# Performance work log

Hardware: AMD Instinct MI355X
Metric: run time of the kernel (lower is better)

## Reference

```python
import jax, jax.numpy as jnp
import numpy as np

LATENT = 256; INPUT = 128; NUNITS = 256; DEC_OUT = 128
NTRAJ = 256; NTP = 512
INTERP = 2  # hard-coded in the original forward

def _mlp_sig(x, w1, b1, w2, b2):
    return jax.nn.sigmoid(jnp.tanh(x @ w1 + b1) @ w2 + b2)

def _mlp_lin(x, w1, b1, w2, b2):
    return jnp.tanh(x @ w1 + b1) @ w2 + b2

def _gru_step(y, yt, x, ug, ugt, rg, ns):
    # x: [N, 2*INPUT]; first half = features, second half = observation mask channels
    xh = x[:, :INPUT]
    yc = jnp.concatenate([y, xh], axis=-1)                 # [N, LATENT+INPUT]
    u = _mlp_sig(yc, *ug)
    ut = _mlp_sig(yc, *ugt)
    r = _mlp_sig(yc, *rg)
    new_state = _mlp_lin(jnp.concatenate([y * r, xh], axis=-1), *ns)
    new_y = (1.0 - u) * new_state + u * y
    new_yt = (1.0 - ut) * new_state + ut * yt
    mask = (jnp.sum(x[:, INPUT:], axis=-1, keepdims=True) > 0).astype(x.dtype)
    return mask * new_y + (1.0 - mask) * y, mask * new_yt + (1.0 - mask) * yt

def setup_inputs():
    key = jax.random.key(0)
    ks = iter(jax.random.split(key, 32))
    def p(shape):
        return jax.random.normal(next(ks), shape, dtype=jnp.float32) * 0.05
    d = {}
    d["data"] = jax.random.normal(next(ks), (NTRAJ, NTP, 2 * INPUT), dtype=jnp.float32)
    dts = jax.random.uniform(next(ks), (NTRAJ, NTP), dtype=jnp.float32) + 0.1
    d["time_steps"] = jnp.cumsum(dts, axis=1)              # strictly increasing times
    gin = LATENT + INPUT
    for name in ("ug", "ugt", "rg", "rgt", "ns"):
        d[name + "_w1"] = p((gin, NUNITS)); d[name + "_b1"] = jnp.zeros((NUNITS,), jnp.float32)
        d[name + "_w2"] = p((NUNITS, LATENT)); d[name + "_b2"] = jnp.zeros((LATENT,), jnp.float32)
    d["dk_w1"] = p((LATENT, LATENT)); d["dk_b1"] = jnp.zeros((LATENT,), jnp.float32)
    d["dk_w2"] = p((LATENT, 1)); d["dk_b2"] = jnp.zeros((1,), jnp.float32)
    d["dec_w"] = p((LATENT, DEC_OUT)); d["dec_b"] = jnp.zeros((DEC_OUT,), jnp.float32)
    return d

def reference(data, time_steps,
              ug_w1, ug_b1, ug_w2, ug_b2,
              ugt_w1, ugt_b1, ugt_w2, ugt_b2,
              rg_w1, rg_b1, rg_w2, rg_b2,
              rgt_w1, rgt_b1, rgt_w2, rgt_b2,
              ns_w1, ns_b1, ns_w2, ns_b2,
              dk_w1, dk_b1, dk_w2, dk_b2,
              dec_w, dec_b):
    # Note: reset_gate_target (rgt_*) is computed but never used in the original forward.
    ug = (ug_w1, ug_b1, ug_w2, ug_b2)
    ugt = (ugt_w1, ugt_b1, ugt_w2, ugt_b2)
    rg = (rg_w1, rg_b1, rg_w2, rg_b2)
    ns = (ns_w1, ns_b1, ns_w2, ns_b2)
    n_traj = data.shape[0]
    lin = jnp.linspace(0.0, 1.0, INTERP + 1, dtype=data.dtype)  # [3]
    y0 = jnp.zeros((n_traj, LATENT), data.dtype)
    # step i=0: no decay interpolation, yi_decay = prev_y (zeros)
    y, yt = _gru_step(y0, y0, data[:, 0, :], ug, ugt, rg, ns)
    dts = time_steps[:, 1:] - time_steps[:, :-1]                # [N, T-1]
    xs = jnp.moveaxis(data[:, 1:, :], 1, 0)                     # [T-1, N, 2I]

    def step(carry, inp):
        y, yt = carry
        x, dt = inp
        decay = jax.nn.relu(jax.nn.relu(y @ dk_w1 + dk_b1) @ dk_w2 + dk_b2)  # [N,1]
        e = jnp.exp(-decay * (dt[:, None] * lin[None, :]))                   # [N,3]
        ydec = yt[:, None, :] + (y - yt)[:, None, :] * e[:, :, None]         # [N,3,L]
        vol = jnp.mean(ydec[:, :-1, :] @ dec_w + dec_b, axis=-2)             # [N,D]
        y2, yt2 = _gru_step(ydec[:, -1, :], yt, x, ug, ugt, rg, ns)
        return (y2, yt2), vol

    (y, yt), vols = jax.lax.scan(step, (y, yt), (xs, dts.T))
    prev_y = y[None, :, :]                       # [1, N, L]
    volume_dt = jnp.transpose(vols, (1, 0, 2))   # [N, T-1, D]
    return prev_y, volume_dt, dts
```

## Files before the change

### kernel.cpp

```cpp
#include <hip/hip_runtime.h>
#include <hip/hip_fp16.h>

#define NTRAJ   256
#define NTP     512
#define NSTEPS  511
#define LATENT  256
#define INPUT   128
#define DEC_OUT 128

#define OUT_VOL ((size_t)NTRAJ * LATENT)
#define OUT_DTS (OUT_VOL + (size_t)NTRAJ * NSTEPS * DEC_OUT)

#define WU_UG1  0
#define WU_UG2  49152
#define WU_UGT1 81920
#define WU_UGT2 131072
#define WU_RG1  163840
#define WU_RG2  212992
#define WU_NS1  245760
#define WU_NS2  294912
#define WU_DK1  327680
#define WU_DEC  360448
#define WU_TOT  376832

typedef _Float16 h2_t __attribute__((ext_vector_type(2)));
union U32H2 { unsigned int u; h2_t h; };

__device__ __forceinline__ float dot2f(unsigned int wu, unsigned int xu, float acc) {
#if defined(__has_builtin) && __has_builtin(__builtin_amdgcn_fdot2)
    U32H2 a, b; a.u = wu; b.u = xu;
    return __builtin_amdgcn_fdot2(a.h, b.h, acc, false);
#else
    U32H2 a, b; a.u = wu; b.u = xu;
    return acc + (float)a.h.x * (float)b.h.x + (float)a.h.y * (float)b.h.y;
#endif
}

__device__ __forceinline__ float wred(float v) {
    #pragma unroll
    for (int off = 32; off; off >>= 1) v += __shfl_down(v, off, 64);
    return v;
}
__device__ __forceinline__ float fast_sigmoid(float x) { return 1.0f / (1.0f + __expf(-x)); }
__device__ __forceinline__ float fast_tanh(float x) {
    float e = __expf(2.0f * x);
    return 1.0f - 2.0f / (e + 1.0f);
}
__device__ __forceinline__ unsigned int packpair(float v) {
    float vn = __shfl_xor(v, 1, 64);
    U32H2 r; r.h.x = (_Float16)v; r.h.y = (_Float16)vn;
    return r.u;
}

extern "C" __global__ void __launch_bounds__(256)
convert_w(const float* __restrict__ ug_w1, const float* __restrict__ ug_w2,
          const float* __restrict__ ugt_w1, const float* __restrict__ ugt_w2,
          const float* __restrict__ rg_w1, const float* __restrict__ rg_w2,
          const float* __restrict__ ns_w1, const float* __restrict__ ns_w2,
          const float* __restrict__ dk_w1, const float* __restrict__ dec_w,
          unsigned int* __restrict__ ws)
{
    const int i = blockIdx.x * 256 + threadIdx.x;
    const float* s; int o; int cbits;
    if      (i < WU_UG2)  { s = ug_w1;  o = i;           cbits = 8; }
    else if (i < WU_UGT1) { s = ug_w2;  o = i - WU_UG2;  cbits = 8; }
    else if (i < WU_UGT2) { s = ugt_w1; o = i - WU_UGT1; cbits = 8; }
    else if (i < WU_RG1)  { s = ugt_w2; o = i - WU_UGT2; cbits = 8; }
    else if (i < WU_RG2)  { s = rg_w1;  o = i - WU_RG1;  cbits = 8; }
    else if (i < WU_NS1)  { s = rg_w2;  o = i - WU_RG2;  cbits = 8; }
    else if (i < WU_NS2)  { s = ns_w1;  o = i - WU_NS1;  cbits = 8; }
    else if (i < WU_DK1)  { s = ns_w2;  o = i - WU_NS2;  cbits = 8; }
    else if (i < WU_DEC)  { s = dk_w1;  o = i - WU_DK1;  cbits = 8; }
    else                  { s = dec_w;  o = i - WU_DEC;  cbits = 7; }
    const int C  = 1 << cbits;
    const int kp = o >> cbits;
    const int c  = o & (C - 1);
    const float v0 = s[(2 * kp) * C + c];
    const float v1 = s[(2 * kp + 1) * C + c];
    const unsigned int h0 = __half_as_ushort(__float2half(v0));
    const unsigned int h1 = __half_as_ushort(__float2half(v1));
    ws[i] = h0 | (h1 << 16);
}

extern "C" __global__ void __launch_bounds__(512, 2)
rnn_decay_kernel3(const float* __restrict__ data, const float* __restrict__ ts,
                  const float* __restrict__ ug_b1, const float* __restrict__ ug_b2,
                  const float* __restrict__ ugt_b1, const float* __restrict__ ugt_b2,
                  const float* __restrict__ rg_b1, const float* __restrict__ rg_b2,
                  const float* __restrict__ ns_b1, const float* __restrict__ ns_b2,
                  const float* __restrict__ dk_b1, const float* __restrict__ dk_w2,
                  const float* __restrict__ dk_b2, const float* __restrict__ dec_b,
                  const unsigned int* __restrict__ wsu, float* __restrict__ out)
{
    __shared__ __align__(16) float s_part[8192];
    __shared__ unsigned int s_in_h[192];
    __shared__ unsigned int s_ns_h[192];
    __shared__ unsigned int s_y_h[128];
    __shared__ unsigned int s_a_h[128];
    __shared__ unsigned int s_b_h[128];
    __shared__ unsigned int s_c_h[128];
    __shared__ unsigned int s_v_h[128];
    __shared__ float s_ut[256];
    __shared__ float s_red[8];

    const int tid  = threadIdx.x;
    const int w    = tid >> 6;
    const int lane = tid & 63;
    const int c    = tid & 255;
    const int cl4  = lane << 2;
    const int traj = blockIdx.x;

    const unsigned int* UG1  = wsu + WU_UG1;  const unsigned int* UG2  = wsu + WU_UG2;
    const unsigned int* UGT1 = wsu + WU_UGT1; const unsigned int* UGT2 = wsu + WU_UGT2;
    const unsigned int* RG1  = wsu + WU_RG1;  const unsigned int* RG2  = wsu + WU_RG2;
    const unsigned int* NS1  = wsu + WU_NS1;  const unsigned int* NS2  = wsu + WU_NS2;
    const unsigned int* DK1  = wsu + WU_DK1;  const unsigned int* DECW = wsu + WU_DEC;

    const float* dbase = data + (size_t)traj * NTP * (2 * INPUT);
    const float* tbase = ts + (size_t)traj * NTP;
    float* vol_out = out + OUT_VOL + (size_t)traj * NSTEPS * DEC_OUT;
    float* dts_out = out + OUT_DTS + (size_t)traj * NSTEPS;

    if (tid < 256)
        for (int t = c; t < NSTEPS; t += 256)
            dts_out[t] = tbase[t + 1] - tbase[t];

    float r_y = 0.f, r_yt = 0.f;

    for (int t = -1; t < NSTEPS; ++t) {
        const bool first = (t < 0);

        if (tid < 256) {
            const float xv = first ? dbase[c] : dbase[(size_t)(t + 1) * 256 + c];
            float mv = (c >= 128) ? xv : 0.f;
            mv = wred(mv);
            if (lane == 0) s_red[w] = mv;
            if (c < 128) {
                const unsigned int px = packpair(xv);
                if (!(lane & 1)) { s_in_h[128 + (c >> 1)] = px; s_ns_h[128 + (c >> 1)] = px; }
            }
            if (first && !(lane & 1)) s_in_h[c >> 1] = 0u;
        }

        float r_ydec = 0.f, r_u = 0.f, r_r = 0.f;
        bool maskv;

        if (!first) {
            float4 aD = make_float4(0, 0, 0, 0);
            const int kp0 = w << 4;
            #pragma unroll 4
            for (int i = 0; i < 16; ++i) {
                const unsigned int x = s_y_h[kp0 + i];
                const uint4 wv = *(const uint4*)(DK1 + (size_t)(kp0 + i) * 256 + cl4);
                aD.x = dot2f(wv.x, x, aD.x); aD.y = dot2f(wv.y, x, aD.y);
                aD.z = dot2f(wv.z, x, aD.z); aD.w = dot2f(wv.w, x, aD.w);
            }
            *(float4*)(s_part + (w << 8) + cl4) = aD;
            __syncthreads();
            if (tid < 256) {
                float v = dk_b1[c];
                #pragma unroll
                for (int i = 0; i < 8; ++i) v += s_part[(i << 8) + c];
                v = fmaxf(v, 0.f);
                float pv = wred(v * dk_w2[c]);
                if (lane == 0) s_red[4 + w] = pv;
            }
            __syncthreads();
            const float decay = fmaxf(s_red[4] + s_red[5] + s_red[6] + s_red[7] + dk_b2[0], 0.f);
            maskv = (s_red[0] + s_red[1] + s_red[2] + s_red[3]) > 0.f;
            if (tid < 256) {
                const float dt = tbase[t + 1] - tbase[t];
                const float diff = r_y - r_yt;
                const float ef = __expf(-decay * dt);
                const float eh = __expf(-0.5f * decay * dt);
                r_ydec = r_yt + diff * ef;
                const float vol = 0.5f * (r_y + r_yt + diff * eh);
                const unsigned int pd = packpair(r_ydec);
                const unsigned int pvv = packpair(vol);
                if (!(lane & 1)) { s_in_h[c >> 1] = pd; s_v_h[c >> 1] = pvv; }
            }
            __syncthreads();
        } else {
            __syncthreads();
            maskv = (s_red[0] + s_red[1] + s_red[2] + s_red[3]) > 0.f;
        }

        if (!first) {
            float4 aE = make_float4(0, 0, 0, 0);
            const int hh = lane >> 5, cl = (lane & 31) << 2;
            const int kpb = (w << 4) + hh;
            #pragma unroll 4
            for (int i = 0; i < 8; ++i) {
                const int kp = kpb + (i << 1);
                const uint4 wv = *(const uint4*)(DECW + (size_t)kp * 128 + cl);
                const unsigned int x = s_v_h[kp];
                aE.x = dot2f(wv.x, x, aE.x); aE.y = dot2f(wv.y, x, aE.y);
                aE.z = dot2f(wv.z, x, aE.z); aE.w = dot2f(wv.w, x, aE.w);
            }
            *(float4*)(s_part + 6144 + ((w << 1) + hh) * 128 + cl) = aE;
        }
        {
            float4 aA = make_float4(0, 0, 0, 0), aB = aA, aC = aA;
            const int kp0 = w * 24;
            #pragma unroll 4
            for (int i = 0; i < 24; ++i) {
                const int kp = kp0 + i;
                const unsigned int x = s_in_h[kp];
                const uint4 wa = *(const uint4*)(UG1  + (size_t)kp * 256 + cl4);
                const uint4 wb = *(const uint4*)(UGT1 + (size_t)kp * 256 + cl4);
                const uint4 wc = *(const uint4*)(RG1  + (size_t)kp * 256 + cl4);
                aA.x = dot2f(wa.x, x, aA.x); aA.y = dot2f(wa.y, x, aA.y);
                aA.z = dot2f(wa.z, x, aA.z); aA.w = dot2f(wa.w, x, aA.w);
                aB.x = dot2f(wb.x, x, aB.x); aB.y = dot2f(wb.y, x, aB.y);
                aB.z = dot2f(wb.z, x, aB.z); aB.w = dot2f(wb.w, x, aB.w);
                aC.x = dot2f(wc.x, x, aC.x); aC.y = dot2f(wc.y, x, aC.y);
                aC.z = dot2f(wc.z, x, aC.z); aC.w = dot2f(wc.w, x, aC.w);
            }
            *(float4*)(s_part + (w << 8) + cl4)          = aA;
            *(float4*)(s_part + 2048 + (w << 8) + cl4)   = aB;
            *(float4*)(s_part + 4096 + (w << 8) + cl4)   = aC;
        }
        __syncthreads();
        {
            const int s = tid >> 8;
            float v = (s ? ugt_b1 : ug_b1)[c];
            const float* pb = s_part + (s ? 2048 : 0) + c;
            #pragma unroll
            for (int i = 0; i < 8; ++i) v += pb[i << 8];
            v = fast_tanh(v);
            const unsigned int pk = packpair(v);
            if (!(lane & 1)) (s ? s_b_h : s_a_h)[c >> 1] = pk;
            if (tid < 256) {
                float v2 = rg_b1[c];
                const float* pb2 = s_part + 4096 + c;
                #pragma unroll
                for (int i = 0; i < 8; ++i) v2 += pb2[i << 8];
                v2 = fast_tanh(v2);
                const unsigned int pk2 = packpair(v2);
                if (!(lane & 1)) s_c_h[c >> 1] = pk2;
            }
            if (!first && tid < 128) {
                float vd = dec_b[tid];
                const float* pbd = s_part + 6144 + tid;
                #pragma unroll
                for (int i = 0; i < 16; ++i) vd += pbd[i << 7];
                vol_out[(size_t)t * DEC_OUT + tid] = vd;
            }
        }
        __syncthreads();

        {
            float4 aA = make_float4(0, 0, 0, 0), aB = aA, aC = aA;
            const int kp0 = w << 4;
            #pragma unroll 4
            for (int i = 0; i < 16; ++i) {
                const int kp = kp0 + i;
                const unsigned int xa = s_a_h[kp];
                const unsigned int xb = s_b_h[kp];
                const unsigned int xc = s_c_h[kp];
                const uint4 wa = *(const uint4*)(UG2  + (size_t)kp * 256 + cl4);
                const uint4 wb = *(const uint4*)(UGT2 + (size_t)kp * 256 + cl4);
                const uint4 wc = *(const uint4*)(RG2  + (size_t)kp * 256 + cl4);
                aA.x = dot2f(wa.x, xa, aA.x); aA.y = dot2f(wa.y, xa, aA.y);
                aA.z = dot2f(wa.z, xa, aA.z); aA.w = dot2f(wa.w, xa, aA.w);
                aB.x = dot2f(wb.x, xb, aB.x); aB.y = dot2f(wb.y, xb, aB.y);
                aB.z = dot2f(wb.z, xb, aB.z); aB.w = dot2f(wb.w, xb, aB.w);
                aC.x = dot2f(wc.x, xc, aC.x); aC.y = dot2f(wc.y, xc, aC.y);
                aC.z = dot2f(wc.z, xc, aC.z); aC.w = dot2f(wc.w, xc, aC.w);
            }
            *(float4*)(s_part + (w << 8) + cl4)          = aA;
            *(float4*)(s_part + 2048 + (w << 8) + cl4)   = aB;
            *(float4*)(s_part + 4096 + (w << 8) + cl4)   = aC;
        }
        __syncthreads();
        {
            const int s = tid >> 8;
            float v = (s ? ugt_b2 : ug_b2)[c];
            const float* pb = s_part + (s ? 2048 : 0) + c;
            #pragma unroll
            for (int i = 0; i < 8; ++i) v += pb[i << 8];
            v = fast_sigmoid(v);
            if (s) s_ut[c] = v; else r_u = v;
            if (tid < 256) {
                float v2 = rg_b2[c];
                const float* pb2 = s_part + 4096 + c;
                #pragma unroll
                for (int i = 0; i < 8; ++i) v2 += pb2[i << 8];
                r_r = fast_sigmoid(v2);
                const unsigned int pk = packpair(r_ydec * r_r);
                if (!(lane & 1)) s_ns_h[c >> 1] = pk;
            }
        }
        __syncthreads();

        {
            float4 aA = make_float4(0, 0, 0, 0);
            const int kp0 = w * 24;
            #pragma unroll 4
            for (int i = 0; i < 24; ++i) {
                const int kp = kp0 + i;
                const unsigned int x = s_ns_h[kp];
                const uint4 wa = *(const uint4*)(NS1 + (size_t)kp * 256 + cl4);
                aA.x = dot2f(wa.x, x, aA.x); aA.y = dot2f(wa.y, x, aA.y);
                aA.z = dot2f(wa.z, x, aA.z); aA.w = dot2f(wa.w, x, aA.w);
            }
            *(float4*)(s_part + (w << 8) + cl4) = aA;
        }
        __syncthreads();
        if (tid < 256) {
            float v = ns_b1[c];
            #pragma unroll
            for (int i = 0; i < 8; ++i) v += s_part[(i << 8) + c];
            v = fast_tanh(v);
            const unsigned int pk = packpair(v);
            if (!(lane & 1)) s_a_h[c >> 1] = pk;
        }
        __syncthreads();

        {
            float4 aA = make_float4(0, 0, 0, 0);
            const int kp0 = w << 4;
            #pragma unroll 4
            for (int i = 0; i < 16; ++i) {
                const int kp = kp0 + i;
                const unsigned int x = s_a_h[kp];
                const uint4 wa = *(const uint4*)(NS2 + (size_t)kp * 256 + cl4);
                aA.x = dot2f(wa.x, x, aA.x); aA.y = dot2f(wa.y, x, aA.y);
                aA.z = dot2f(wa.z, x, aA.z); aA.w = dot2f(wa.w, x, aA.w);
            }
            *(float4*)(s_part + (w << 8) + cl4) = aA;
        }
        __syncthreads();
        if (tid < 256) {
            float nsv = ns_b2[c];
            #pragma unroll
            for (int i = 0; i < 8; ++i) nsv += s_part[(i << 8) + c];
            const float u = r_u, ut = s_ut[c];
            const float ny  = (1.f - u)  * nsv + u  * r_ydec;
            const float nyt = (1.f - ut) * nsv + ut * r_yt;
            r_y  = maskv ? ny  : r_ydec;
            r_yt = maskv ? nyt : r_yt;
            const unsigned int pk = packpair(r_y);
            if (!(lane & 1)) s_y_h[c >> 1] = pk;
        }
        __syncthreads();
    }

    if (tid < 256)
        out[(size_t)traj * 256 + c] = r_y;
}

extern "C" void kernel_launch(void* const* d_in, const int* in_sizes, int n_in,
                              void* d_out, int out_size, void* d_ws, size_t ws_size,
                              hipStream_t stream) {
    const float* data   = (const float*)d_in[0];
    const float* ts     = (const float*)d_in[1];
    const float* ug_w1  = (const float*)d_in[2];
    const float* ug_b1  = (const float*)d_in[3];
    const float* ug_w2  = (const float*)d_in[4];
    const float* ug_b2  = (const float*)d_in[5];
    const float* ugt_w1 = (const float*)d_in[6];
    const float* ugt_b1 = (const float*)d_in[7];
    const float* ugt_w2 = (const float*)d_in[8];
    const float* ugt_b2 = (const float*)d_in[9];
    const float* rg_w1  = (const float*)d_in[10];
    const float* rg_b1  = (const float*)d_in[11];
    const float* rg_w2  = (const float*)d_in[12];
    const float* rg_b2  = (const float*)d_in[13];
    const float* ns_w1  = (const float*)d_in[18];
    const float* ns_b1  = (const float*)d_in[19];
    const float* ns_w2  = (const float*)d_in[20];
    const float* ns_b2  = (const float*)d_in[21];
    const float* dk_w1  = (const float*)d_in[22];
    const float* dk_b1  = (const float*)d_in[23];
    const float* dk_w2  = (const float*)d_in[24];
    const float* dk_b2  = (const float*)d_in[25];
    const float* dec_w  = (const float*)d_in[26];
    const float* dec_b  = (const float*)d_in[27];

    unsigned int* wsu = (unsigned int*)d_ws;

    convert_w<<<WU_TOT / 256, 256, 0, stream>>>(ug_w1, ug_w2, ugt_w1, ugt_w2,
                                                rg_w1, rg_w2, ns_w1, ns_w2,
                                                dk_w1, dec_w, wsu);

    rnn_decay_kernel3<<<NTRAJ, 512, 0, stream>>>(
        data, ts, ug_b1, ug_b2, ugt_b1, ugt_b2, rg_b1, rg_b2, ns_b1, ns_b2,
        dk_b1, dk_w2, dk_b2, dec_b, wsu, (float*)d_out);
}
```

Baseline: 7.585 ms.

## Replace shared-memory partial reductions with intra-wave shuffle reductions per output column

Each matvec is now split so each wave owns 32 output columns and its 8 lane groups split the K dimension. Partial sums are combined with xor-shuffle butterflies instead of being written to a 32KB shared scratch array and re-summed. This removes the separate reduction phases and about half of the __syncthreads per timestep, and frees a large shared buffer. In exchange it adds shuffle traffic, and the activation work after each reduction is done redundantly by every lane group rather than spread across threads.

Result: slower. 8.042 ms (+6.0%).

```diff
diff --git a/kernel.cpp b/kernel.cpp
--- a/kernel.cpp
+++ b/kernel.cpp
@@ -50,6 +50,16 @@
     float vn = __shfl_xor(v, 1, 64);
     U32H2 r; r.h.x = (_Float16)v; r.h.y = (_Float16)vn;
     return r.u;
+}
+__device__ __forceinline__ unsigned int pk2(float a, float b) {
+    U32H2 r; r.h.x = (_Float16)a; r.h.y = (_Float16)b; return r.u;
+}
+__device__ __forceinline__ float4 bfly4(float4 v, int m) {
+    v.x += __shfl_xor(v.x, m, 64);
+    v.y += __shfl_xor(v.y, m, 64);
+    v.z += __shfl_xor(v.z, m, 64);
+    v.w += __shfl_xor(v.w, m, 64);
+    return v;
 }
 
 extern "C" __global__ void __launch_bounds__(256)
@@ -82,8 +92,12 @@
     ws[i] = h0 | (h1 << 16);
 }
 
+#define DOT1(acc, wv, xv) { \
+    acc.x = dot2f((wv).x, (xv), acc.x); acc.y = dot2f((wv).y, (xv), acc.y); \
+    acc.z = dot2f((wv).z, (xv), acc.z); acc.w = dot2f((wv).w, (xv), acc.w); }
+
 extern "C" __global__ void __launch_bounds__(512, 2)
-rnn_decay_kernel3(const float* __restrict__ data, const float* __restrict__ ts,
+rnn_decay_kernel4(const float* __restrict__ data, const float* __restrict__ ts,
                   const float* __restrict__ ug_b1, const float* __restrict__ ug_b2,
                   const float* __restrict__ ugt_b1, const float* __restrict__ ugt_b2,
                   const float* __restrict__ rg_b1, const float* __restrict__ rg_b2,
@@ -92,22 +106,25 @@
                   const float* __restrict__ dk_b2, const float* __restrict__ dec_b,
                   const unsigned int* __restrict__ wsu, float* __restrict__ out)
 {
-    __shared__ __align__(16) float s_part[8192];
-    __shared__ unsigned int s_in_h[192];
-    __shared__ unsigned int s_ns_h[192];
-    __shared__ unsigned int s_y_h[128];
-    __shared__ unsigned int s_a_h[128];
-    __shared__ unsigned int s_b_h[128];
-    __shared__ unsigned int s_c_h[128];
-    __shared__ unsigned int s_v_h[128];
-    __shared__ float s_ut[256];
-    __shared__ float s_red[8];
+    __shared__ __align__(16) unsigned int s_in_h[192];
+    __shared__ __align__(16) unsigned int s_ns_h[192];
+    __shared__ __align__(16) unsigned int s_y_h[128];
+    __shared__ __align__(16) unsigned int s_a_h[128];
+    __shared__ __align__(16) unsigned int s_b_h[128];
+    __shared__ __align__(16) unsigned int s_c_h[128];
+    __shared__ __align__(16) unsigned int s_v_h[128];
+    __shared__ float s_red[12];
 
     const int tid  = threadIdx.x;
     const int w    = tid >> 6;
     const int lane = tid & 63;
     const int c    = tid & 255;
-    const int cl4  = lane << 2;
+    const int sl   = lane >> 3;
+    const int g    = lane & 7;
+    const int c0   = (w << 5) + (g << 2);
+    const int h2b  = c0 >> 1;
+    const int sld  = lane >> 2;
+    const int c0d  = (w << 4) + ((lane & 3) << 2);
     const int traj = blockIdx.x;
 
     const unsigned int* UG1  = wsu + WU_UG1;  const unsigned int* UG2  = wsu + WU_UG2;
@@ -122,232 +139,225 @@
     float* dts_out = out + OUT_DTS + (size_t)traj * NSTEPS;
 
     if (tid < 256)
-        for (int t = c; t < NSTEPS; t += 256)
-            dts_out[t] = tbase[t + 1] - tbase[t];
-
-    float r_y = 0.f, r_yt = 0.f;
+        for (int t0 = c; t0 < NSTEPS; t0 += 256)
+            dts_out[t0] = tbase[t0 + 1] - tbase[t0];
+
+    const float4 ugb1v  = *(const float4*)(ug_b1  + c0);
+    const float4 ugtb1v = *(const float4*)(ugt_b1 + c0);
+    const float4 rgb1v  = *(const float4*)(rg_b1  + c0);
+    const float4 nsb1v  = *(const float4*)(ns_b1  + c0);
+    const float4 ugb2v  = *(const float4*)(ug_b2  + c0);
+    const float4 ugtb2v = *(const float4*)(ugt_b2 + c0);
+    const float4 rgb2v  = *(const float4*)(rg_b2  + c0);
+    const float4 nsb2v  = *(const float4*)(ns_b2  + c0);
+    const float4 dkb1v  = *(const float4*)(dk_b1  + c0);
+    const float4 dkw2v  = *(const float4*)(dk_w2  + c0);
+    const float4 decbv  = *(const float4*)(dec_b  + c0d);
+    const float  dkb2s  = dk_b2[0];
+
+    float4 y4  = make_float4(0.f, 0.f, 0.f, 0.f);
+    float4 yt4 = y4;
 
     for (int t = -1; t < NSTEPS; ++t) {
         const bool first = (t < 0);
 
+        float dt_t = 0.f;
+        if (!first) dt_t = tbase[t + 1] - tbase[t];
+        float xval = 0.f;
+        if (tid < 256)
+            xval = first ? dbase[c] : dbase[(size_t)(t + 1) * 256 + c];
+
+        if (!first) {
+            float4 aD = make_float4(0.f, 0.f, 0.f, 0.f);
+            #pragma unroll 4
+            for (int i = 0; i < 16; ++i) {
+                const int kp = sl + (i << 3);
+                const unsigned int xv = s_y_h[kp];
+                const uint4 wv = *(const uint4*)(DK1 + (size_t)kp * 256 + c0);
+                DOT1(aD, wv, xv);
+            }
+            aD = bfly4(aD, 8); aD = bfly4(aD, 16); aD = bfly4(aD, 32);
+            float sdk = fmaxf(aD.x + dkb1v.x, 0.f) * dkw2v.x
+                      + fmaxf(aD.y + dkb1v.y, 0.f) * dkw2v.y
+                      + fmaxf(aD.z + dkb1v.z, 0.f) * dkw2v.z
+                      + fmaxf(aD.w + dkb1v.w, 0.f) * dkw2v.w;
+            sdk += __shfl_xor(sdk, 1, 64);
+            sdk += __shfl_xor(sdk, 2, 64);
+            sdk += __shfl_xor(sdk, 4, 64);
+            if (lane == 0) s_red[4 + w] = sdk;
+        }
         if (tid < 256) {
-            const float xv = first ? dbase[c] : dbase[(size_t)(t + 1) * 256 + c];
-            float mv = (c >= 128) ? xv : 0.f;
+            float mv = (c >= 128) ? xval : 0.f;
             mv = wred(mv);
             if (lane == 0) s_red[w] = mv;
             if (c < 128) {
-                const unsigned int px = packpair(xv);
+                const unsigned int px = packpair(xval);
                 if (!(lane & 1)) { s_in_h[128 + (c >> 1)] = px; s_ns_h[128 + (c >> 1)] = px; }
             }
             if (first && !(lane & 1)) s_in_h[c >> 1] = 0u;
         }
-
-        float r_ydec = 0.f, r_u = 0.f, r_r = 0.f;
-        bool maskv;
-
+        __syncthreads();
+
+        const bool maskv = (s_red[0] + s_red[1] + s_red[2] + s_red[3]) > 0.f;
+        float4 ydec4 = make_float4(0.f, 0.f, 0.f, 0.f);
         if (!first) {
-            float4 aD = make_float4(0, 0, 0, 0);
-            const int kp0 = w << 4;
+            const float decay = fmaxf(s_red[4] + s_red[5] + s_red[6] + s_red[7]
+                                    + s_red[8] + s_red[9] + s_red[10] + s_red[11]
+                                    + dkb2s, 0.f);
+            const float ef = __expf(-decay * dt_t);
+            const float eh = __expf(-0.5f * decay * dt_t);
+            float4 vol4;
+            ydec4.x = yt4.x + (y4.x - yt4.x) * ef;
+            ydec4.y = yt4.y + (y4.y - yt4.y) * ef;
+            ydec4.z = yt4.z + (y4.z - yt4.z) * ef;
+            ydec4.w = yt4.w + (y4.w - yt4.w) * ef;
+            vol4.x = 0.5f * (y4.x + yt4.x + (y4.x - yt4.x) * eh);
+            vol4.y = 0.5f * (y4.y + yt4.y + (y4.y - yt4.y) * eh);
+            vol4.z = 0.5f * (y4.z + yt4.z + (y4.z - yt4.z) * eh);
+            vol4.w = 0.5f * (y4.w + yt4.w + (y4.w - yt4.w) * eh);
+            if (!sl) {
+                uint2 pd; pd.x = pk2(ydec4.x, ydec4.y); pd.y = pk2(ydec4.z, ydec4.w);
+                uint2 pv; pv.x = pk2(vol4.x, vol4.y);   pv.y = pk2(vol4.z, vol4.w);
+                *(uint2*)(s_in_h + h2b) = pd;
+                *(uint2*)(s_v_h + h2b)  = pv;
+            }
+        }
+        __syncthreads();
+
+        if (!first) {
+            float4 aE = make_float4(0.f, 0.f, 0.f, 0.f);
+            #pragma unroll 4
+            for (int i = 0; i < 8; ++i) {
+                const int kp = sld + (i << 4);
+                const unsigned int xv = s_v_h[kp];
+                const uint4 wv = *(const uint4*)(DECW + (size_t)kp * 128 + c0d);
+                DOT1(aE, wv, xv);
+            }
+            aE = bfly4(aE, 4); aE = bfly4(aE, 8); aE = bfly4(aE, 16); aE = bfly4(aE, 32);
+            if (sld == 0) {
+                float4 o;
+                o.x = aE.x + decbv.x; o.y = aE.y + decbv.y;
+                o.z = aE.z + decbv.z; o.w = aE.w + decbv.w;
+                *(float4*)(vol_out + (size_t)t * DEC_OUT + c0d) = o;
+            }
+        }
+        {
+            float4 aA = make_float4(0.f, 0.f, 0.f, 0.f), aB = aA, aC = aA;
+            #pragma unroll 4
+            for (int i = 0; i < 24; ++i) {
+                const int kp = sl + (i << 3);
+                const unsigned int xv = s_in_h[kp];
+                const uint4 wa = *(const uint4*)(UG1  + (size_t)kp * 256 + c0);
+                const uint4 wb = *(const uint4*)(UGT1 + (size_t)kp * 256 + c0);
+                const uint4 wc = *(const uint4*)(RG1  + (size_t)kp * 256 + c0);
+                DOT1(aA, wa, xv); DOT1(aB, wb, xv); DOT1(aC, wc, xv);
+            }
+            aA = bfly4(aA, 8); aA = bfly4(aA, 16); aA = bfly4(aA, 32);
+            aB = bfly4(aB, 8); aB = bfly4(aB, 16); aB = bfly4(aB, 32);
+            aC = bfly4(aC, 8); aC = bfly4(aC, 16); aC = bfly4(aC, 32);
+            if (!sl) {
+                uint2 pa, pb, pc;
+                pa.x = pk2(fast_tanh(aA.x + ugb1v.x),  fast_tanh(aA.y + ugb1v.y));
+                pa.y = pk2(fast_tanh(aA.z + ugb1v.z),  fast_tanh(aA.w + ugb1v.w));
+                pb.x = pk2(fast_tanh(aB.x + ugtb1v.x), fast_tanh(aB.y + ugtb1v.y));
+                pb.y = pk2(fast_tanh(aB.z + ugtb1v.z), fast_tanh(aB.w + ugtb1v.w));
+                pc.x = pk2(fast_tanh(aC.x + rgb1v.x),  fast_tanh(aC.y + rgb1v.y));
+                pc.y = pk2(fast_tanh(aC.z + rgb1v.z),  fast_tanh(aC.w + rgb1v.w));
+                *(uint2*)(s_a_h + h2b) = pa;
+                *(uint2*)(s_b_h + h2b) = pb;
+                *(uint2*)(s_c_h + h2b) = pc;
+            }
+        }
+        __syncthreads();
+
+        float4 u4, ut4;
+        {
+            float4 aA = make_float4(0.f, 0.f, 0.f, 0.f), aB = aA, aC = aA;
             #pragma unroll 4
             for (int i = 0; i < 16; ++i) {
-                const unsigned int x = s_y_h[kp0 + i];
-                const uint4 wv = *(const uint4*)(DK1 + (size_t)(kp0 + i) * 256 + cl4);
-                aD.x = dot2f(wv.x, x, aD.x); aD.y = dot2f(wv.y, x, aD.y);
-                aD.z = dot2f(wv.z, x, aD.z); aD.w = dot2f(wv.w, x, aD.w);
-            }
-            *(float4*)(s_part + (w << 8) + cl4) = aD;
-            __syncthreads();
-            if (tid < 256) {
-                float v = dk_b1[c];
-                #pragma unroll
-                for (int i = 0; i < 8; ++i) v += s_part[(i << 8) + c];
-                v = fmaxf(v, 0.f);
-                float pv = wred(v * dk_w2[c]);
-                if (lane == 0) s_red[4 + w] = pv;
-            }
-            __syncthreads();
-            const float decay = fmaxf(s_red[4] + s_red[5] + s_red[6] + s_red[7] + dk_b2[0], 0.f);
-            maskv = (s_red[0] + s_red[1] + s_red[2] + s_red[3]) > 0.f;
-            if (tid < 256) {
-                const float dt = tbase[t + 1] - tbase[t];
-                const float diff = r_y - r_yt;
-                const float ef = __expf(-decay * dt);
-                const float eh = __expf(-0.5f * decay * dt);
-                r_ydec = r_yt + diff * ef;
-                const float vol = 0.5f * (r_y + r_yt + diff * eh);
-                const unsigned int pd = packpair(r_ydec);
-                const unsigned int pvv = packpair(vol);
-                if (!(lane & 1)) { s_in_h[c >> 1] = pd; s_v_h[c >> 1] = pvv; }
-            }
-            __syncthreads();
-        } else {
-            __syncthreads();
-            maskv = (s_red[0] + s_red[1] + s_red[2] + s_red[3]) > 0.f;
-        }
-
-        if (!first) {
-            float4 aE = make_float4(0, 0, 0, 0);
-            const int hh = lane >> 5, cl = (lane & 31) << 2;
-            const int kpb = (w << 4) + hh;
-            #pragma unroll 4
-            for (int i = 0; i < 8; ++i) {
-                const int kp = kpb + (i << 1);
-                const uint4 wv = *(const uint4*)(DECW + (size_t)kp * 128 + cl);
-                const unsigned int x = s_v_h[kp];
-                aE.x = dot2f(wv.x, x, aE.x); aE.y = dot2f(wv.y, x, aE.y);
-                aE.z = dot2f(wv.z, x, aE.z); aE.w = dot2f(wv.w, x, aE.w);
-            }
-            *(float4*)(s_part + 6144 + ((w << 1) + hh) * 128 + cl) = aE;
-        }
-        {
-            float4 aA = make_float4(0, 0, 0, 0), aB = aA, aC = aA;
-            const int kp0 = w * 24;
-            #pragma unroll 4
-            for (int i = 0; i < 24; ++i) {
-                const int kp = kp0 + i;
-                const unsigned int x = s_in_h[kp];
-                const uint4 wa = *(const uint4*)(UG1  + (size_t)kp * 256 + cl4);
-                const uint4 wb = *(const uint4*)(UGT1 + (size_t)kp * 256 + cl4);
-                const uint4 wc = *(const uint4*)(RG1  + (size_t)kp * 256 + cl4);
-                aA.x = dot2f(wa.x, x, aA.x); aA.y = dot2f(wa.y, x, aA.y);
-                aA.z = dot2f(wa.z, x, aA.z); aA.w = dot2f(wa.w, x, aA.w);
-                aB.x = dot2f(wb.x, x, aB.x); aB.y = dot2f(wb.y, x, aB.y);
-                aB.z = dot2f(wb.z, x, aB.z); aB.w = dot2f(wb.w, x, aB.w);
-                aC.x = dot2f(wc.x, x, aC.x); aC.y = dot2f(wc.y, x, aC.y);
-                aC.z = dot2f(wc.z, x, aC.z); aC.w = dot2f(wc.w, x, aC.w);
-            }
-            *(float4*)(s_part + (w << 8) + cl4)          = aA;
-            *(float4*)(s_part + 2048 + (w << 8) + cl4)   = aB;
-            *(float4*)(s_part + 4096 + (w << 8) + cl4)   = aC;
-        }
-        __syncthreads();
-        {
-            const int s = tid >> 8;
-            float v = (s ? ugt_b1 : ug_b1)[c];
-            const float* pb = s_part + (s ? 2048 : 0) + c;
-            #pragma unroll
-            for (int i = 0; i < 8; ++i) v += pb[i << 8];
-            v = fast_tanh(v);
-            const unsigned int pk = packpair(v);
-            if (!(lane & 1)) (s ? s_b_h : s_a_h)[c >> 1] = pk;
-            if (tid < 256) {
-                float v2 = rg_b1[c];
-                const float* pb2 = s_part + 4096 + c;
-                #pragma unroll
-                for (int i = 0; i < 8; ++i) v2 += pb2[i << 8];
-                v2 = fast_tanh(v2);
-                const unsigned int pk2 = packpair(v2);
-                if (!(lane & 1)) s_c_h[c >> 1] = pk2;
-            }
-            if (!first && tid < 128) {
-                float vd = dec_b[tid];
-                const float* pbd = s_part + 6144 + tid;
-                #pragma unroll
-                for (int i = 0; i < 16; ++i) vd += pbd[i << 7];
-                vol_out[(size_t)t * DEC_OUT + tid] = vd;
-            }
-        }
-        __syncthreads();
-
-        {
-            float4 aA = make_float4(0, 0, 0, 0), aB = aA, aC = aA;
-            const int kp0 = w << 4;
-            #pragma unroll 4
-            for (int i = 0; i < 16; ++i) {
-                const int kp = kp0 + i;
+                const int kp = sl + (i << 3);
                 const unsigned int xa = s_a_h[kp];
                 const unsigned int xb = s_b_h[kp];
                 const unsigned int xc = s_c_h[kp];
-                const uint4 wa = *(const uint4*)(UG2  + (size_t)kp * 256 + cl4);
-                const uint4 wb = *(const uint4*)(UGT2 + (size_t)kp * 256 + cl4);
-                const uint4 wc = *(const uint4*)(RG2  + (size_t)kp * 256 + cl4);
-                aA.x = dot2f(wa.x, xa, aA.x); aA.y = dot2f(wa.y, xa, aA.y);
-                aA.z = dot2f(wa.z, xa, aA.z); aA.w = dot2f(wa.w, xa, aA.w);
-                aB.x = dot2f(wb.x, xb, aB.x); aB.y = dot2f(wb.y, xb, aB.y);
-                aB.z = dot2f(wb.z, xb, aB.z); aB.w = dot2f(wb.w, xb, aB.w);
-                aC.x = dot2f(wc.x, xc, aC.x); aC.y = dot2f(wc.y, xc, aC.y);
-                aC.z = dot2f(wc.z, xc, aC.z); aC.w = dot2f(wc.w, xc, aC.w);
-            }
-            *(float4*)(s_part + (w << 8) + cl4)          = aA;
-            *(float4*)(s_part + 2048 + (w << 8) + cl4)   = aB;
-            *(float4*)(s_part + 4096 + (w << 8) + cl4)   = aC;
-        }
-        __syncthreads();
+                const uint4 wa = *(const uint4*)(UG2  + (size_t)kp * 256 + c0);
+                const uint4 wb = *(const uint4*)(UGT2 + (size_t)kp * 256 + c0);
+                const uint4 wc = *(const uint4*)(RG2  + (size_t)kp * 256 + c0);
+                DOT1(aA, wa, xa); DOT1(aB, wb, xb); DOT1(aC, wc, xc);
+            }
+            aA = bfly4(aA, 8); aA = bfly4(aA, 16); aA = bfly4(aA, 32);
+            aB = bfly4(aB, 8); aB = bfly4(aB, 16); aB = bfly4(aB, 32);
+            aC = bfly4(aC, 8); aC = bfly4(aC, 16); aC = bfly4(aC, 32);
+            u4.x  = fast_sigmoid(aA.x + ugb2v.x);  u4.y  = fast_sigmoid(aA.y + ugb2v.y);
+            u4.z  = fast_sigmoid(aA.z + ugb2v.z);  u4.w  = fast_sigmoid(aA.w + ugb2v.w);
+            ut4.x = fast_sigmoid(aB.x + ugtb2v.x); ut4.y = fast_sigmoid(aB.y + ugtb2v.y);
+            ut4.z = fast_sigmoid(aB.z + ugtb2v.z); ut4.w = fast_sigmoid(aB.w + ugtb2v.w);
+            const float rx = fast_sigmoid(aC.x + rgb2v.x);
+            const float ry = fast_sigmoid(aC.y + rgb2v.y);
+            const float rz = fast_sigmoid(aC.z + rgb2v.z);
+            const float rw = fast_sigmoid(aC.w + rgb2v.w);
+            if (!sl) {
+                uint2 pn;
+                pn.x = pk2(ydec4.x * rx, ydec4.y * ry);
+                pn.y = pk2(ydec4.z * rz, ydec4.w * rw);
+                *(uint2*)(s_ns_h + h2b) = pn;
+            }
+        }
+        __syncthreads();
+
         {
-            const int s = tid >> 8;
-            float v = (s ? ugt_b2 : ug_b2)[c];
-            const float* pb = s_part + (s ? 2048 : 0) + c;
-            #pragma unroll
-            for (int i = 0; i < 8; ++i) v += pb[i << 8];
-            v = fast_sigmoid(v);
-            if (s) s_ut[c] = v; else r_u = v;
-            if (tid < 256) {
-                float v2 = rg_b2[c];
-                const float* pb2 = s_part + 4096 + c;
-                #pragma unroll
-                for (int i = 0; i < 8; ++i) v2 += pb2[i << 8];
-                r_r = fast_sigmoid(v2);
-                const unsigned int pk = packpair(r_ydec * r_r);
-                if (!(lane & 1)) s_ns_h[c >> 1] = pk;
+            float4 aA = make_float4(0.f, 0.f, 0.f, 0.f);
+            #pragma unroll 4
+            for (int i = 0; i < 24; ++i) {
+                const int kp = sl + (i << 3);
+                const unsigned int xv = s_ns_h[kp];
+                const uint4 wa = *(const uint4*)(NS1 + (size_t)kp * 256 + c0);
+                DOT1(aA, wa, xv);
+            }
+            aA = bfly4(aA, 8); aA = bfly4(aA, 16); aA = bfly4(aA, 32);
+            if (!sl) {
+                uint2 ph;
+                ph.x = pk2(fast_tanh(aA.x + nsb1v.x), fast_tanh(aA.y + nsb1v.y));
+                ph.y = pk2(fast_tanh(aA.z + nsb1v.z), fast_tanh(aA.w + nsb1v.w));
+                *(uint2*)(s_a_h + h2b) = ph;
             }
         }
         __syncthreads();
 
         {
-            float4 aA = make_float4(0, 0, 0, 0);
-            const int kp0 = w * 24;
-            #pragma unroll 4
-            for (int i = 0; i < 24; ++i) {
-                const int kp = kp0 + i;
-                const unsigned int x = s_ns_h[kp];
-                const uint4 wa = *(const uint4*)(NS1 + (size_t)kp * 256 + cl4);
-                aA.x = dot2f(wa.x, x, aA.x); aA.y = dot2f(wa.y, x, aA.y);
-                aA.z = dot2f(wa.z, x, aA.z); aA.w = dot2f(wa.w, x, aA.w);
-            }
-            *(float4*)(s_part + (w << 8) + cl4) = aA;
-        }
-        __syncthreads();
-        if (tid < 256) {
-            float v = ns_b1[c];
-            #pragma unroll
-            for (int i = 0; i < 8; ++i) v += s_part[(i << 8) + c];
-            v = fast_tanh(v);
-            const unsigned int pk = packpair(v);
-            if (!(lane & 1)) s_a_h[c >> 1] = pk;
-        }
-        __syncthreads();
-
-        {
-            float4 aA = make_float4(0, 0, 0, 0);
-            const int kp0 = w << 4;
+            float4 aA = make_float4(0.f, 0.f, 0.f, 0.f);
             #pragma unroll 4
             for (int i = 0; i < 16; ++i) {
-                const int kp = kp0 + i;
-                const unsigned int x = s_a_h[kp];
-                const uint4 wa = *(const uint4*)(NS2 + (size_t)kp * 256 + cl4);
-                aA.x = dot2f(wa.x, x, aA.x); aA.y = dot2f(wa.y, x, aA.y);
-                aA.z = dot2f(wa.z, x, aA.z); aA.w = dot2f(wa.w, x, aA.w);
-            }
-            *(float4*)(s_part + (w << 8) + cl4) = aA;
-        }
-        __syncthreads();
-        if (tid < 256) {
-            float nsv = ns_b2[c];
-            #pragma unroll
-            for (int i = 0; i < 8; ++i) nsv += s_part[(i << 8) + c];
-            const float u = r_u, ut = s_ut[c];
-            const float ny  = (1.f - u)  * nsv + u  * r_ydec;
-            const float nyt = (1.f - ut) * nsv + ut * r_yt;
-            r_y  = maskv ? ny  : r_ydec;
-            r_yt = maskv ? nyt : r_yt;
-            const unsigned int pk = packpair(r_y);
-            if (!(lane & 1)) s_y_h[c >> 1] = pk;
+                const int kp = sl + (i << 3);
+                const unsigned int xv = s_a_h[kp];
+                const uint4 wa = *(const uint4*)(NS2 + (size_t)kp * 256 + c0);
+                DOT1(aA, wa, xv);
+            }
+            aA = bfly4(aA, 8); aA = bfly4(aA, 16); aA = bfly4(aA, 32);
+            const float nx = aA.x + nsb2v.x, ny_ = aA.y + nsb2v.y;
+            const float nz = aA.z + nsb2v.z, nw = aA.w + nsb2v.w;
+            const float yx = (1.f - u4.x) * nx  + u4.x * ydec4.x;
+            const float yy = (1.f - u4.y) * ny_ + u4.y * ydec4.y;
+            const float yz = (1.f - u4.z) * nz  + u4.z * ydec4.z;
+            const float yw = (1.f - u4.w) * nw  + u4.w * ydec4.w;
+            const float tx = (1.f - ut4.x) * nx  + ut4.x * yt4.x;
+            const float ty = (1.f - ut4.y) * ny_ + ut4.y * yt4.y;
+            const float tz = (1.f - ut4.z) * nz  + ut4.z * yt4.z;
+            const float tw = (1.f - ut4.w) * nw  + ut4.w * yt4.w;
+            y4.x  = maskv ? yx : ydec4.x;  y4.y  = maskv ? yy : ydec4.y;
+            y4.z  = maskv ? yz : ydec4.z;  y4.w  = maskv ? yw : ydec4.w;
+            yt4.x = maskv ? tx : yt4.x;    yt4.y = maskv ? ty : yt4.y;
+            yt4.z = maskv ? tz : yt4.z;    yt4.w = maskv ? tw : yt4.w;
+            if (!sl) {
+                uint2 py;
+                py.x = pk2(y4.x, y4.y); py.y = pk2(y4.z, y4.w);
+                *(uint2*)(s_y_h + h2b) = py;
+            }
         }
         __syncthreads();
     }
 
-    if (tid < 256)
-        out[(size_t)traj * 256 + c] = r_y;
+    if (!sl)
+        *(float4*)(out + (size_t)traj * 256 + c0) = y4;
 }
 
 extern "C" void kernel_launch(void* const* d_in, const int* in_sizes, int n_in,
@@ -384,7 +394,7 @@
                                                 rg_w1, rg_w2, ns_w1, ns_w2,
                                                 dk_w1, dec_w, wsu);
 
-    rnn_decay_kernel3<<<NTRAJ, 512, 0, stream>>>(
+    rnn_decay_kernel4<<<NTRAJ, 512, 0, stream>>>(
         data, ts, ug_b1, ug_b2, ugt_b1, ugt_b2, rg_b1, rg_b2, ns_b1, ns_b2,
         dk_b1, dk_w2, dk_b2, dec_b, wsu, (float*)d_out);
 }
```

## Double block to 1024 threads, halving per-wave K-slice in every matvec

Applied to the files above, without the earlier changes.

The per-trajectory recurrent kernel now launches 1024 threads (16 waves) instead of 512. Each matvec stage gives every wave half as many K rows, and the cross-wave reductions sum 16 partials instead of 8. The bias/activation phase now spreads the three gate reductions and the decoder output across four 256-thread groups instead of doubling up. This aims to cut per-step latency on a serial, latency-bound scan by adding more memory parallelism per CU. In exchange it uses more shared memory, makes each reduction longer, and makes barriers with 16 waves more expensive.

Result: no change. 7.624 ms (+0.5%).

```diff
diff --git a/kernel.cpp b/kernel.cpp
--- a/kernel.cpp
+++ b/kernel.cpp
@@ -82,8 +82,12 @@
     ws[i] = h0 | (h1 << 16);
 }
 
-extern "C" __global__ void __launch_bounds__(512, 2)
-rnn_decay_kernel3(const float* __restrict__ data, const float* __restrict__ ts,
+#define DOT1(acc, wv, xv) { \
+    acc.x = dot2f((wv).x, (xv), acc.x); acc.y = dot2f((wv).y, (xv), acc.y); \
+    acc.z = dot2f((wv).z, (xv), acc.z); acc.w = dot2f((wv).w, (xv), acc.w); }
+
+extern "C" __global__ void __launch_bounds__(1024, 4)
+rnn_decay_kernel7(const float* __restrict__ data, const float* __restrict__ ts,
                   const float* __restrict__ ug_b1, const float* __restrict__ ug_b2,
                   const float* __restrict__ ugt_b1, const float* __restrict__ ugt_b2,
                   const float* __restrict__ rg_b1, const float* __restrict__ rg_b2,
@@ -92,14 +96,15 @@
                   const float* __restrict__ dk_b2, const float* __restrict__ dec_b,
                   const unsigned int* __restrict__ wsu, float* __restrict__ out)
 {
-    __shared__ __align__(16) float s_part[8192];
-    __shared__ unsigned int s_in_h[192];
-    __shared__ unsigned int s_ns_h[192];
-    __shared__ unsigned int s_y_h[128];
-    __shared__ unsigned int s_a_h[128];
-    __shared__ unsigned int s_b_h[128];
-    __shared__ unsigned int s_c_h[128];
-    __shared__ unsigned int s_v_h[128];
+    __shared__ __align__(16) float s_part[12288];
+    __shared__ __align__(16) float s_partd[4096];
+    __shared__ __align__(16) unsigned int s_in_h[192];
+    __shared__ __align__(16) unsigned int s_ns_h[192];
+    __shared__ __align__(16) unsigned int s_y_h[128];
+    __shared__ __align__(16) unsigned int s_a_h[128];
+    __shared__ __align__(16) unsigned int s_b_h[128];
+    __shared__ __align__(16) unsigned int s_c_h[128];
+    __shared__ __align__(16) unsigned int s_v_h[128];
     __shared__ float s_ut[256];
     __shared__ float s_red[8];
 
@@ -122,60 +127,65 @@
     float* dts_out = out + OUT_DTS + (size_t)traj * NSTEPS;
 
     if (tid < 256)
-        for (int t = c; t < NSTEPS; t += 256)
-            dts_out[t] = tbase[t + 1] - tbase[t];
+        for (int t0 = c; t0 < NSTEPS; t0 += 256)
+            dts_out[t0] = tbase[t0 + 1] - tbase[t0];
 
     float r_y = 0.f, r_yt = 0.f;
+
+    const int kp12 = w * 12;
+    const int kp8  = w << 3;
 
     for (int t = -1; t < NSTEPS; ++t) {
         const bool first = (t < 0);
 
         if (tid < 256) {
-            const float xv = first ? dbase[c] : dbase[(size_t)(t + 1) * 256 + c];
-            float mv = (c >= 128) ? xv : 0.f;
+            const float xval = first ? dbase[c] : dbase[(size_t)(t + 1) * 256 + c];
+            float mv = (c >= 128) ? xval : 0.f;
             mv = wred(mv);
             if (lane == 0) s_red[w] = mv;
             if (c < 128) {
-                const unsigned int px = packpair(xv);
+                const unsigned int px = packpair(xval);
                 if (!(lane & 1)) { s_in_h[128 + (c >> 1)] = px; s_ns_h[128 + (c >> 1)] = px; }
             }
             if (first && !(lane & 1)) s_in_h[c >> 1] = 0u;
         }
 
-        float r_ydec = 0.f, r_u = 0.f, r_r = 0.f;
+        float r_ydec = 0.f, r_u = 0.f;
         bool maskv;
 
         if (!first) {
-            float4 aD = make_float4(0, 0, 0, 0);
-            const int kp0 = w << 4;
-            #pragma unroll 4
-            for (int i = 0; i < 16; ++i) {
-                const unsigned int x = s_y_h[kp0 + i];
-                const uint4 wv = *(const uint4*)(DK1 + (size_t)(kp0 + i) * 256 + cl4);
-                aD.x = dot2f(wv.x, x, aD.x); aD.y = dot2f(wv.y, x, aD.y);
-                aD.z = dot2f(wv.z, x, aD.z); aD.w = dot2f(wv.w, x, aD.w);
-            }
-            *(float4*)(s_part + (w << 8) + cl4) = aD;
+            {
+                float4 aD = make_float4(0.f, 0.f, 0.f, 0.f);
+                #pragma unroll 4
+                for (int i = 0; i < 8; ++i) {
+                    const int kp = kp8 + i;
+                    const unsigned int xv = s_y_h[kp];
+                    const uint4 wv = *(const uint4*)(DK1 + (size_t)kp * 256 + cl4);
+                    DOT1(aD, wv, xv);
+                }
+                *(float4*)(s_part + (w << 8) + cl4) = aD;
+            }
             __syncthreads();
             if (tid < 256) {
                 float v = dk_b1[c];
                 #pragma unroll
-                for (int i = 0; i < 8; ++i) v += s_part[(i << 8) + c];
+                for (int i = 0; i < 16; ++i) v += s_part[(i << 8) + c];
                 v = fmaxf(v, 0.f);
-                float pv = wred(v * dk_w2[c]);
+                const float pv = wred(v * dk_w2[c]);
                 if (lane == 0) s_red[4 + w] = pv;
             }
             __syncthreads();
-            const float decay = fmaxf(s_red[4] + s_red[5] + s_red[6] + s_red[7] + dk_b2[0], 0.f);
             maskv = (s_red[0] + s_red[1] + s_red[2] + s_red[3]) > 0.f;
             if (tid < 256) {
+                const float decay = fmaxf(s_red[4] + s_red[5] + s_red[6] + s_red[7]
+                                        + dk_b2[0], 0.f);
                 const float dt = tbase[t + 1] - tbase[t];
                 const float diff = r_y - r_yt;
                 const float ef = __expf(-decay * dt);
                 const float eh = __expf(-0.5f * decay * dt);
                 r_ydec = r_yt + diff * ef;
                 const float vol = 0.5f * (r_y + r_yt + diff * eh);
-                const unsigned int pd = packpair(r_ydec);
+                const unsigned int pd  = packpair(r_ydec);
                 const unsigned int pvv = packpair(vol);
                 if (!(lane & 1)) { s_in_h[c >> 1] = pd; s_v_h[c >> 1] = pvv; }
             }
@@ -186,123 +196,115 @@
         }
 
         if (!first) {
-            float4 aE = make_float4(0, 0, 0, 0);
+            float4 aE = make_float4(0.f, 0.f, 0.f, 0.f);
             const int hh = lane >> 5, cl = (lane & 31) << 2;
-            const int kpb = (w << 4) + hh;
-            #pragma unroll 4
-            for (int i = 0; i < 8; ++i) {
+            const int kpb = kp8 + hh;
+            #pragma unroll
+            for (int i = 0; i < 4; ++i) {
                 const int kp = kpb + (i << 1);
                 const uint4 wv = *(const uint4*)(DECW + (size_t)kp * 128 + cl);
-                const unsigned int x = s_v_h[kp];
-                aE.x = dot2f(wv.x, x, aE.x); aE.y = dot2f(wv.y, x, aE.y);
-                aE.z = dot2f(wv.z, x, aE.z); aE.w = dot2f(wv.w, x, aE.w);
-            }
-            *(float4*)(s_part + 6144 + ((w << 1) + hh) * 128 + cl) = aE;
-        }
-        {
-            float4 aA = make_float4(0, 0, 0, 0), aB = aA, aC = aA;
-            const int kp0 = w * 24;
+                const unsigned int xv = s_v_h[kp];
+                DOT1(aE, wv, xv);
+            }
+            *(float4*)(s_partd + ((w << 1) + hh) * 128 + cl) = aE;
+        }
+
+        {
+            float4 aA = make_float4(0.f, 0.f, 0.f, 0.f), aB = aA, aC = aA;
             #pragma unroll 4
-            for (int i = 0; i < 24; ++i) {
-                const int kp = kp0 + i;
-                const unsigned int x = s_in_h[kp];
+            for (int i = 0; i < 12; ++i) {
+                const int kp = kp12 + i;
+                const unsigned int xv = s_in_h[kp];
                 const uint4 wa = *(const uint4*)(UG1  + (size_t)kp * 256 + cl4);
                 const uint4 wb = *(const uint4*)(UGT1 + (size_t)kp * 256 + cl4);
                 const uint4 wc = *(const uint4*)(RG1  + (size_t)kp * 256 + cl4);
-                aA.x = dot2f(wa.x, x, aA.x); aA.y = dot2f(wa.y, x, aA.y);
-                aA.z = dot2f(wa.z, x, aA.z); aA.w = dot2f(wa.w, x, aA.w);
-                aB.x = dot2f(wb.x, x, aB.x); aB.y = dot2f(wb.y, x, aB.y);
-                aB.z = dot2f(wb.z, x, aB.z); aB.w = dot2f(wb.w, x, aB.w);
-                aC.x = dot2f(wc.x, x, aC.x); aC.y = dot2f(wc.y, x, aC.y);
-                aC.z = dot2f(wc.z, x, aC.z); aC.w = dot2f(wc.w, x, aC.w);
+                DOT1(aA, wa, xv); DOT1(aB, wb, xv); DOT1(aC, wc, xv);
             }
             *(float4*)(s_part + (w << 8) + cl4)          = aA;
-            *(float4*)(s_part + 2048 + (w << 8) + cl4)   = aB;
-            *(float4*)(s_part + 4096 + (w << 8) + cl4)   = aC;
+            *(float4*)(s_part + 4096 + (w << 8) + cl4)   = aB;
+            *(float4*)(s_part + 8192 + (w << 8) + cl4)   = aC;
         }
         __syncthreads();
         {
             const int s = tid >> 8;
-            float v = (s ? ugt_b1 : ug_b1)[c];
-            const float* pb = s_part + (s ? 2048 : 0) + c;
-            #pragma unroll
-            for (int i = 0; i < 8; ++i) v += pb[i << 8];
-            v = fast_tanh(v);
-            const unsigned int pk = packpair(v);
-            if (!(lane & 1)) (s ? s_b_h : s_a_h)[c >> 1] = pk;
-            if (tid < 256) {
-                float v2 = rg_b1[c];
-                const float* pb2 = s_part + 4096 + c;
-                #pragma unroll
-                for (int i = 0; i < 8; ++i) v2 += pb2[i << 8];
-                v2 = fast_tanh(v2);
-                const unsigned int pk2 = packpair(v2);
-                if (!(lane & 1)) s_c_h[c >> 1] = pk2;
-            }
-            if (!first && tid < 128) {
-                float vd = dec_b[tid];
-                const float* pbd = s_part + 6144 + tid;
-                #pragma unroll
-                for (int i = 0; i < 16; ++i) vd += pbd[i << 7];
-                vol_out[(size_t)t * DEC_OUT + tid] = vd;
-            }
-        }
-        __syncthreads();
-
-        {
-            float4 aA = make_float4(0, 0, 0, 0), aB = aA, aC = aA;
-            const int kp0 = w << 4;
+            if (s == 0) {
+                float v = ug_b1[c];
+                #pragma unroll
+                for (int i = 0; i < 16; ++i) v += s_part[(i << 8) + c];
+                v = fast_tanh(v);
+                const unsigned int pk = packpair(v);
+                if (!(lane & 1)) s_a_h[c >> 1] = pk;
+            } else if (s == 1) {
+                float v = ugt_b1[c];
+                #pragma unroll
+                for (int i = 0; i < 16; ++i) v += s_part[4096 + (i << 8) + c];
+                v = fast_tanh(v);
+                const unsigned int pk = packpair(v);
+                if (!(lane & 1)) s_b_h[c >> 1] = pk;
+            } else if (s == 2) {
+                float v = rg_b1[c];
+                #pragma unroll
+                for (int i = 0; i < 16; ++i) v += s_part[8192 + (i << 8) + c];
+                v = fast_tanh(v);
+                const unsigned int pk = packpair(v);
+                if (!(lane & 1)) s_c_h[c >> 1] = pk;
+            } else if (!first && c < 128) {
+                float vd = dec_b[c];
+                #pragma unroll
+                for (int i = 0; i < 32; ++i) vd += s_partd[(i << 7) + c];
+                vol_out[(size_t)t * DEC_OUT + c] = vd;
+            }
+        }
+        __syncthreads();
+
+        {
+            float4 aA = make_float4(0.f, 0.f, 0.f, 0.f), aB = aA, aC = aA;
             #pragma unroll 4
-            for (int i = 0; i < 16; ++i) {
-                const int kp = kp0 + i;
+            for (int i = 0; i < 8; ++i) {
+                const int kp = kp8 + i;
                 const unsigned int xa = s_a_h[kp];
                 const unsigned int xb = s_b_h[kp];
                 const unsigned int xc = s_c_h[kp];
                 const uint4 wa = *(const uint4*)(UG2  + (size_t)kp * 256 + cl4);
                 const uint4 wb = *(const uint4*)(UGT2 + (size_t)kp * 256 + cl4);
                 const uint4 wc = *(const uint4*)(RG2  + (size_t)kp * 256 + cl4);
-                aA.x = dot2f(wa.x, xa, aA.x); aA.y = dot2f(wa.y, xa, aA.y);
-                aA.z = dot2f(wa.z, xa, aA.z); aA.w = dot2f(wa.w, xa, aA.w);
-                aB.x = dot2f(wb.x, xb, aB.x); aB.y = dot2f(wb.y, xb, aB.y);
-                aB.z = dot2f(wb.z, xb, aB.z); aB.w = dot2f(wb.w, xb, aB.w);
-                aC.x = dot2f(wc.x, xc, aC.x); aC.y = dot2f(wc.y, xc, aC.y);
-                aC.z = dot2f(wc.z, xc, aC.z); aC.w = dot2f(wc.w, xc, aC.w);
+                DOT1(aA, wa, xa); DOT1(aB, wb, xb); DOT1(aC, wc, xc);
             }
             *(float4*)(s_part + (w << 8) + cl4)          = aA;
-            *(float4*)(s_part + 2048 + (w << 8) + cl4)   = aB;
-            *(float4*)(s_part + 4096 + (w << 8) + cl4)   = aC;
+            *(float4*)(s_part + 4096 + (w << 8) + cl4)   = aB;
+            *(float4*)(s_part + 8192 + (w << 8) + cl4)   = aC;
         }
         __syncthreads();
         {
             const int s = tid >> 8;
-            float v = (s ? ugt_b2 : ug_b2)[c];
-            const float* pb = s_part + (s ? 2048 : 0) + c;
-            #pragma unroll
-            for (int i = 0; i < 8; ++i) v += pb[i << 8];
-            v = fast_sigmoid(v);
-            if (s) s_ut[c] = v; else r_u = v;
-            if (tid < 256) {
+            if (s == 0) {
+                float v = ug_b2[c];
+                #pragma unroll
+                for (int i = 0; i < 16; ++i) v += s_part[(i << 8) + c];
+                r_u = fast_sigmoid(v);
                 float v2 = rg_b2[c];
-                const float* pb2 = s_part + 4096 + c;
-                #pragma unroll
-                for (int i = 0; i < 8; ++i) v2 += pb2[i << 8];
-                r_r = fast_sigmoid(v2);
-                const unsigned int pk = packpair(r_ydec * r_r);
+                #pragma unroll
+                for (int i = 0; i < 16; ++i) v2 += s_part[8192 + (i << 8) + c];
+                const float rr = fast_sigmoid(v2);
+                const unsigned int pk = packpair(r_ydec * rr);
                 if (!(lane & 1)) s_ns_h[c >> 1] = pk;
-            }
-        }
-        __syncthreads();
-
-        {
-            float4 aA = make_float4(0, 0, 0, 0);
-            const int kp0 = w * 24;
+            } else if (s == 1) {
+                float v = ugt_b2[c];
+                #pragma unroll
+                for (int i = 0; i < 16; ++i) v += s_part[4096 + (i << 8) + c];
+                s_ut[c] = fast_sigmoid(v);
+            }
+        }
+        __syncthreads();
+
+        {
+            float4 aA = make_float4(0.f, 0.f, 0.f, 0.f);
             #pragma unroll 4
-            for (int i = 0; i < 24; ++i) {
-                const int kp = kp0 + i;
-                const unsigned int x = s_ns_h[kp];
+            for (int i = 0; i < 12; ++i) {
+                const int kp = kp12 + i;
+                const unsigned int xv = s_ns_h[kp];
                 const uint4 wa = *(const uint4*)(NS1 + (size_t)kp * 256 + cl4);
-                aA.x = dot2f(wa.x, x, aA.x); aA.y = dot2f(wa.y, x, aA.y);
-                aA.z = dot2f(wa.z, x, aA.z); aA.w = dot2f(wa.w, x, aA.w);
+                DOT1(aA, wa, xv);
             }
             *(float4*)(s_part + (w << 8) + cl4) = aA;
         }
@@ -310,7 +312,7 @@
         if (tid < 256) {
             float v = ns_b1[c];
             #pragma unroll
-            for (int i = 0; i < 8; ++i) v += s_part[(i << 8) + c];
+            for (int i = 0; i < 16; ++i) v += s_part[(i << 8) + c];
             v = fast_tanh(v);
             const unsigned int pk = packpair(v);
             if (!(lane & 1)) s_a_h[c >> 1] = pk;
@@ -318,15 +320,13 @@
         __syncthreads();
 
         {
-            float4 aA = make_float4(0, 0, 0, 0);
-            const int kp0 = w << 4;
+            float4 aA = make_float4(0.f, 0.f, 0.f, 0.f);
             #pragma unroll 4
-            for (int i = 0; i < 16; ++i) {
-                const int kp = kp0 + i;
-                const unsigned int x = s_a_h[kp];
+            for (int i = 0; i < 8; ++i) {
+                const int kp = kp8 + i;
+                const unsigned int xv = s_a_h[kp];
                 const uint4 wa = *(const uint4*)(NS2 + (size_t)kp * 256 + cl4);
-                aA.x = dot2f(wa.x, x, aA.x); aA.y = dot2f(wa.y, x, aA.y);
-                aA.z = dot2f(wa.z, x, aA.z); aA.w = dot2f(wa.w, x, aA.w);
+                DOT1(aA, wa, xv);
             }
             *(float4*)(s_part + (w << 8) + cl4) = aA;
         }
@@ -334,7 +334,7 @@
         if (tid < 256) {
             float nsv = ns_b2[c];
             #pragma unroll
-            for (int i = 0; i < 8; ++i) nsv += s_part[(i << 8) + c];
+            for (int i = 0; i < 16; ++i) nsv += s_part[(i << 8) + c];
             const float u = r_u, ut = s_ut[c];
             const float ny  = (1.f - u)  * nsv + u  * r_ydec;
             const float nyt = (1.f - ut) * nsv + ut * r_yt;
@@ -384,7 +384,7 @@
                                                 rg_w1, rg_w2, ns_w1, ns_w2,
                                                 dk_w1, dec_w, wsu);
 
-    rnn_decay_kernel3<<<NTRAJ, 512, 0, stream>>>(
+    rnn_decay_kernel7<<<NTRAJ, 1024, 0, stream>>>(
         data, ts, ug_b1, ug_b2, ugt_b1, ugt_b2, rg_b1, rg_b2, ns_b1, ns_b2,
         dk_b1, dk_w2, dk_b2, dec_b, wsu, (float*)d_out);
 }
```
